# Optimization experiments

Measured on AMD Instinct MI355X. Metric: run time of the kernel, lower is better.

## Reference

```python
import jax, jax.numpy as jnp
import numpy as np

NSITES, NUP, BATCH = 128, 64, 4096


def _rand_distinct_sorted_idx(key, batch, nsites, nup):
    # per-sample distinct site indices (prefix of a random permutation), sorted
    u = jax.random.uniform(key, (batch, nsites))
    idx = jnp.argsort(u, axis=1)[:, :nup]
    return jnp.sort(idx, axis=1).astype(jnp.int32)


def setup_inputs() -> dict:
    key = jax.random.key(0)
    k1, k2, k3 = jax.random.split(key, 3)
    U = jax.random.normal(k1, (NSITES, NUP), dtype=jnp.float32)
    idx_up = _rand_distinct_sorted_idx(k2, BATCH, NSITES, NUP)
    idx_dn = _rand_distinct_sorted_idx(k3, BATCH, NSITES, NUP)
    return {"U": U, "idx_up": idx_up, "idx_dn": idx_dn}


def reference(U, idx_up, idx_dn):
    # psi(n) = det(n_up * U) * det(n_dn * U), returned in log form
    # gather rows per sample: (B, Nup, Nup)
    sign_up, logabs_up = jnp.linalg.slogdet(U[idx_up, :])
    sign_dn, logabs_dn = jnp.linalg.slogdet(U[idx_dn, :])
    # LogArray product: signs multiply, log-magnitudes add
    return (sign_up * sign_dn, logabs_up + logabs_dn)
```

## Files before the change

kernel.cpp:

```cpp
#include <hip/hip_runtime.h>

#define BATCH 4096
#define N 64

template<int CTRL>
__device__ __forceinline__ float dpp_max_step(float x) {
    int moved = __builtin_amdgcn_update_dpp(0, __float_as_int(x), CTRL, 0xf, 0xf, true);
    return fmaxf(x, __int_as_float(moved));
}

__device__ __forceinline__ float lanebcast(float v, int ps) {
    return __uint_as_float(__builtin_amdgcn_readlane(__float_as_uint(v), ps));
}

__global__ __launch_bounds__(64, 1) void restricted_det_kernel(
    const float* __restrict__ U,
    const int* __restrict__ idx_up,
    const int* __restrict__ idx_dn,
    float* __restrict__ out)
{
    const int lane = threadIdx.x;
    const int wid  = blockIdx.x;

    const int site0 = idx_up[wid * N + lane];
    const int site1 = idx_dn[wid * N + lane];

    float l2sum = 0.0f;
    unsigned int sbits = 0u;
    int inv = 0;

    #pragma unroll 1
    for (int spin = 0; spin < 2; ++spin) {
        const int site = (spin == 0) ? site0 : site1;

        float a[N];
        const float4* __restrict__ row = reinterpret_cast<const float4*>(U + (long)site * N);
        #pragma unroll
        for (int q = 0; q < N / 4; ++q) {
            float4 v = row[q];
            a[4*q+0] = v.x; a[4*q+1] = v.y; a[4*q+2] = v.z; a[4*q+3] = v.w;
        }

        unsigned long long chosen = 0ull;
        bool alive = true;

        #pragma unroll
        for (int k = 0; k < N; ++k) {
            const float key = alive ? __builtin_fabsf(a[k]) : -1.0f;
            float r = key;
            r = dpp_max_step<0x111>(r);
            r = dpp_max_step<0x112>(r);
            r = dpp_max_step<0x114>(r);
            r = dpp_max_step<0x118>(r);
            r = dpp_max_step<0x142>(r);
            r = dpp_max_step<0x143>(r);
            const float mx = __uint_as_float(
                __builtin_amdgcn_readlane(__float_as_uint(r), 63));
            const unsigned long long bal = __ballot(key == mx);
            const int ps = (int)__builtin_ctzll(bal);

            inv += __popcll(chosen >> ps);
            chosen |= (1ull << ps);
            alive = alive && (lane != ps);

            const float pv = lanebcast(a[k], ps);
            sbits ^= __float_as_uint(pv);
            l2sum += __log2f(mx);

            const float rm = __builtin_amdgcn_rcpf(pv);
            const float m  = a[k] * rm;
            #pragma unroll
            for (int j = k + 1; j < N; ++j) {
                const float uv = lanebcast(a[j], ps);
                a[j] = __builtin_fmaf(-m, uv, a[j]);
            }
        }
    }

    if (lane == 0) {
        const float sgn =
            (((sbits >> 31) ^ ((unsigned)inv & 1u)) != 0u) ? -1.0f : 1.0f;
        out[wid] = sgn;
        out[BATCH + wid] = l2sum * 0.69314718055994530942f;
    }
}

extern "C" void kernel_launch(void* const* d_in, const int* in_sizes, int n_in,
                              void* d_out, int out_size, void* d_ws, size_t ws_size,
                              hipStream_t stream) {
    const float* U      = (const float*)d_in[0];
    const int*   idx_up = (const int*)d_in[1];
    const int*   idx_dn = (const int*)d_in[2];
    float* out = (float*)d_out;

    dim3 block(64);
    dim3 grid(BATCH);
    hipLaunchKernelGGL(restricted_det_kernel, grid, block, 0, stream,
                       U, idx_up, idx_dn, out);
}
```

Baseline: 170.6 us.

## Interleave up/down eliminations and pack lane index into pivot max key

Runs the two spin determinants' Gaussian eliminations interleaved in one loop so their independent DPP reductions, readlanes and FMAs can overlap and hide latency. It also packs the lane index into the low bits of the absolute-value key, which removes the ballot/ctz step from pivot selection. The launch bounds are relaxed to allow up to four waves per EU. In exchange, register pressure doubles (two 64-float arrays), which risks spilling, and truncating mantissa bits can change pivot choice on near-ties.

```diff
diff --git a/kernel.cpp b/kernel.cpp
--- a/kernel.cpp
+++ b/kernel.cpp
@@ -4,16 +4,18 @@
 #define N 64
 
 template<int CTRL>
-__device__ __forceinline__ float dpp_max_step(float x) {
-    int moved = __builtin_amdgcn_update_dpp(0, __float_as_int(x), CTRL, 0xf, 0xf, true);
-    return fmaxf(x, __int_as_float(moved));
+__device__ __forceinline__ unsigned dpp_umax(unsigned x) {
+    unsigned moved = (unsigned)__builtin_amdgcn_update_dpp(0, (int)x, CTRL, 0xf, 0xf, true);
+    return (moved > x) ? moved : x;
 }
 
-__device__ __forceinline__ float lanebcast(float v, int ps) {
+__device__ __forceinline__ float lanebcastf(float v, int ps) {
     return __uint_as_float(__builtin_amdgcn_readlane(__float_as_uint(v), ps));
 }
 
-__global__ __launch_bounds__(64, 1) void restricted_det_kernel(
+__global__ __launch_bounds__(64)
+__attribute__((amdgpu_waves_per_eu(1, 4)))
+void restricted_det_kernel(
     const float* __restrict__ U,
     const int* __restrict__ idx_up,
     const int* __restrict__ idx_dn,
@@ -22,58 +24,68 @@
     const int lane = threadIdx.x;
     const int wid  = blockIdx.x;
 
-    const int site0 = idx_up[wid * N + lane];
-    const int site1 = idx_dn[wid * N + lane];
+    const int siteA = idx_up[wid * N + lane];
+    const int siteB = idx_dn[wid * N + lane];
+
+    float aA[N], aB[N];
+    {
+        const float4* __restrict__ ra = reinterpret_cast<const float4*>(U + (long)siteA * N);
+        const float4* __restrict__ rb = reinterpret_cast<const float4*>(U + (long)siteB * N);
+        #pragma unroll
+        for (int q = 0; q < N / 4; ++q) {
+            float4 va = ra[q];
+            float4 vb = rb[q];
+            aA[4*q+0]=va.x; aA[4*q+1]=va.y; aA[4*q+2]=va.z; aA[4*q+3]=va.w;
+            aB[4*q+0]=vb.x; aB[4*q+1]=vb.y; aB[4*q+2]=vb.z; aB[4*q+3]=vb.w;
+        }
+    }
 
     float l2sum = 0.0f;
-    unsigned int sbits = 0u;
+    unsigned sbits = 0u;
     int inv = 0;
+    unsigned long long chosenA = 0ull, chosenB = 0ull;
+    bool aliveA = true, aliveB = true;
 
-    #pragma unroll 1
-    for (int spin = 0; spin < 2; ++spin) {
-        const int site = (spin == 0) ? site0 : site1;
+    #pragma unroll
+    for (int k = 0; k < N; ++k) {
+        unsigned tA = (__float_as_uint(aA[k]) & 0x7FFFFFC0u) | (unsigned)lane;
+        unsigned tB = (__float_as_uint(aB[k]) & 0x7FFFFFC0u) | (unsigned)lane;
+        unsigned rA = aliveA ? tA : 0u;
+        unsigned rB = aliveB ? tB : 0u;
 
-        float a[N];
-        const float4* __restrict__ row = reinterpret_cast<const float4*>(U + (long)site * N);
-        #pragma unroll
-        for (int q = 0; q < N / 4; ++q) {
-            float4 v = row[q];
-            a[4*q+0] = v.x; a[4*q+1] = v.y; a[4*q+2] = v.z; a[4*q+3] = v.w;
-        }
+        rA = dpp_umax<0x111>(rA); rB = dpp_umax<0x111>(rB);
+        rA = dpp_umax<0x112>(rA); rB = dpp_umax<0x112>(rB);
+        rA = dpp_umax<0x114>(rA); rB = dpp_umax<0x114>(rB);
+        rA = dpp_umax<0x118>(rA); rB = dpp_umax<0x118>(rB);
+        rA = dpp_umax<0x142>(rA); rB = dpp_umax<0x142>(rB);
+        rA = dpp_umax<0x143>(rA); rB = dpp_umax<0x143>(rB);
 
-        unsigned long long chosen = 0ull;
-        bool alive = true;
+        const unsigned winA = (unsigned)__builtin_amdgcn_readlane((int)rA, 63);
+        const unsigned winB = (unsigned)__builtin_amdgcn_readlane((int)rB, 63);
+        const int psA = (int)(winA & 63u);
+        const int psB = (int)(winB & 63u);
+
+        inv += __popcll(chosenA >> psA);  chosenA |= (1ull << psA);
+        inv += __popcll(chosenB >> psB);  chosenB |= (1ull << psB);
+        aliveA = aliveA && (lane != psA);
+        aliveB = aliveB && (lane != psB);
+
+        const float pvA = lanebcastf(aA[k], psA);
+        const float pvB = lanebcastf(aB[k], psB);
+        sbits ^= __float_as_uint(pvA) & 0x80000000u;
+        sbits ^= __float_as_uint(pvB) & 0x80000000u;
+        l2sum += __log2f(__builtin_fabsf(pvA));
+        l2sum += __log2f(__builtin_fabsf(pvB));
+
+        const float mA = aA[k] * __builtin_amdgcn_rcpf(pvA);
+        const float mB = aB[k] * __builtin_amdgcn_rcpf(pvB);
 
         #pragma unroll
-        for (int k = 0; k < N; ++k) {
-            const float key = alive ? __builtin_fabsf(a[k]) : -1.0f;
-            float r = key;
-            r = dpp_max_step<0x111>(r);
-            r = dpp_max_step<0x112>(r);
-            r = dpp_max_step<0x114>(r);
-            r = dpp_max_step<0x118>(r);
-            r = dpp_max_step<0x142>(r);
-            r = dpp_max_step<0x143>(r);
-            const float mx = __uint_as_float(
-                __builtin_amdgcn_readlane(__float_as_uint(r), 63));
-            const unsigned long long bal = __ballot(key == mx);
-            const int ps = (int)__builtin_ctzll(bal);
-
-            inv += __popcll(chosen >> ps);
-            chosen |= (1ull << ps);
-            alive = alive && (lane != ps);
-
-            const float pv = lanebcast(a[k], ps);
-            sbits ^= __float_as_uint(pv);
-            l2sum += __log2f(mx);
-
-            const float rm = __builtin_amdgcn_rcpf(pv);
-            const float m  = a[k] * rm;
-            #pragma unroll
-            for (int j = k + 1; j < N; ++j) {
-                const float uv = lanebcast(a[j], ps);
-                a[j] = __builtin_fmaf(-m, uv, a[j]);
-            }
+        for (int j = k + 1; j < N; ++j) {
+            const float uvA = lanebcastf(aA[j], psA);
+            const float uvB = lanebcastf(aB[j], psB);
+            aA[j] = __builtin_fmaf(-mA, uvA, aA[j]);
+            aB[j] = __builtin_fmaf(-mB, uvB, aB[j]);
         }
     }
 
```

After: 186.7 us. 1.09x slower.

## Pack lane index into pivot key and overlap next pivot search with update

Applied to the files above, without the earlier changes.

Pivot selection now packs the lane index into the low 6 bits of the magnitude's bit pattern and does an unsigned max reduction, which removes the ballot and ctz step. Column k+1 is eliminated first so the next pivot's argmax can be issued while the remaining columns are still being updated, hiding the reduction latency behind the rank-1 update FMAs. Truncating the low mantissa bits can make the chosen pivot differ slightly from a true argmax, which may change pivoting on near-ties. The launch bound's minimum-blocks hint is also dropped.

```diff
diff --git a/kernel.cpp b/kernel.cpp
--- a/kernel.cpp
+++ b/kernel.cpp
@@ -4,16 +4,28 @@
 #define N 64
 
 template<int CTRL>
-__device__ __forceinline__ float dpp_max_step(float x) {
-    int moved = __builtin_amdgcn_update_dpp(0, __float_as_int(x), CTRL, 0xf, 0xf, true);
-    return fmaxf(x, __int_as_float(moved));
+__device__ __forceinline__ unsigned dpp_umax(unsigned x) {
+    unsigned moved = (unsigned)__builtin_amdgcn_update_dpp(0, (int)x, CTRL, 0xf, 0xf, true);
+    return (moved > x) ? moved : x;
 }
 
-__device__ __forceinline__ float lanebcast(float v, int ps) {
+__device__ __forceinline__ float lanebcastf(float v, int ps) {
     return __uint_as_float(__builtin_amdgcn_readlane(__float_as_uint(v), ps));
 }
 
-__global__ __launch_bounds__(64, 1) void restricted_det_kernel(
+__device__ __forceinline__ int pivot_argmax(float col, bool alive, int lane) {
+    unsigned t = (__float_as_uint(col) & 0x7FFFFFC0u) | (unsigned)lane;
+    unsigned r = alive ? t : 0u;
+    r = dpp_umax<0x111>(r);
+    r = dpp_umax<0x112>(r);
+    r = dpp_umax<0x114>(r);
+    r = dpp_umax<0x118>(r);
+    r = dpp_umax<0x142>(r);
+    r = dpp_umax<0x143>(r);
+    return (int)(((unsigned)__builtin_amdgcn_readlane((int)r, 63)) & 63u);
+}
+
+__global__ __launch_bounds__(64) void restricted_det_kernel(
     const float* __restrict__ U,
     const int* __restrict__ idx_up,
     const int* __restrict__ idx_dn,
@@ -26,7 +38,7 @@
     const int site1 = idx_dn[wid * N + lane];
 
     float l2sum = 0.0f;
-    unsigned int sbits = 0u;
+    unsigned sbits = 0u;
     int inv = 0;
 
     #pragma unroll 1
@@ -38,43 +50,46 @@
         #pragma unroll
         for (int q = 0; q < N / 4; ++q) {
             float4 v = row[q];
-            a[4*q+0] = v.x; a[4*q+1] = v.y; a[4*q+2] = v.z; a[4*q+3] = v.w;
+            a[4*q+0]=v.x; a[4*q+1]=v.y; a[4*q+2]=v.z; a[4*q+3]=v.w;
         }
 
         unsigned long long chosen = 0ull;
         bool alive = true;
 
+        int ps = pivot_argmax(a[0], alive, lane);
+
         #pragma unroll
-        for (int k = 0; k < N; ++k) {
-            const float key = alive ? __builtin_fabsf(a[k]) : -1.0f;
-            float r = key;
-            r = dpp_max_step<0x111>(r);
-            r = dpp_max_step<0x112>(r);
-            r = dpp_max_step<0x114>(r);
-            r = dpp_max_step<0x118>(r);
-            r = dpp_max_step<0x142>(r);
-            r = dpp_max_step<0x143>(r);
-            const float mx = __uint_as_float(
-                __builtin_amdgcn_readlane(__float_as_uint(r), 63));
-            const unsigned long long bal = __ballot(key == mx);
-            const int ps = (int)__builtin_ctzll(bal);
-
+        for (int k = 0; k < N - 1; ++k) {
             inv += __popcll(chosen >> ps);
             chosen |= (1ull << ps);
             alive = alive && (lane != ps);
 
-            const float pv = lanebcast(a[k], ps);
-            sbits ^= __float_as_uint(pv);
-            l2sum += __log2f(mx);
+            const float pv = lanebcastf(a[k], ps);
+            sbits ^= __float_as_uint(pv) & 0x80000000u;
+            l2sum += __log2f(__builtin_fabsf(pv));
 
-            const float rm = __builtin_amdgcn_rcpf(pv);
-            const float m  = a[k] * rm;
+            const float m = a[k] * __builtin_amdgcn_rcpf(pv);
+
+            {
+                const float uv = lanebcastf(a[k + 1], ps);
+                a[k + 1] = __builtin_fmaf(-m, uv, a[k + 1]);
+            }
+            const int ps_next = pivot_argmax(a[k + 1], alive, lane);
+
             #pragma unroll
-            for (int j = k + 1; j < N; ++j) {
-                const float uv = lanebcast(a[j], ps);
+            for (int j = k + 2; j < N; ++j) {
+                const float uv = lanebcastf(a[j], ps);
                 a[j] = __builtin_fmaf(-m, uv, a[j]);
             }
+
+            ps = ps_next;
         }
+
+        inv += __popcll(chosen >> ps);
+        chosen |= (1ull << ps);
+        const float pv = lanebcastf(a[N - 1], ps);
+        sbits ^= __float_as_uint(pv) & 0x80000000u;
+        l2sum += __log2f(__builtin_fabsf(pv));
     }
 
     if (lane == 0) {
```

New measurement: 160.6 us. 1.06x faster.
